# Optimization experiments

Measured on AMD Instinct MI355X. Metric: run time of the kernel, lower is better.

The kernel has to match this reference:

```python
import jax, jax.numpy as jnp
import numpy as np


def setup_inputs() -> dict:
    key = jax.random.key(0)
    ks = jax.random.split(key, 8)
    B, I, H = 4096, 2048, 2048
    C = I + H
    s = 1.0 / np.sqrt(C)
    return {
        "x": jax.random.normal(ks[0], (B, I), jnp.float32),
        "h": jax.random.normal(ks[1], (B, H), jnp.float32),
        "W_update": jax.random.normal(ks[2], (H, C), jnp.float32) * s,
        "b_update": jax.random.normal(ks[3], (H,), jnp.float32) * s,
        "W_select": jax.random.normal(ks[4], (H, C), jnp.float32) * s,
        "b_select": jax.random.normal(ks[5], (H,), jnp.float32) * s,
        "W_predict": jax.random.normal(ks[6], (H, C), jnp.float32) * s,
        "b_predict": jax.random.normal(ks[7], (H,), jnp.float32) * s,
    }


def reference(x, h, W_update, b_update, W_select, b_select, W_predict, b_predict):
    # combined = [x, h]  -> [B, I+H]
    combined = jnp.concatenate([x, h], axis=1)
    to_update = jax.nn.sigmoid(combined @ W_update.T + b_update)  # [B, H]
    to_select = jax.nn.sigmoid(combined @ W_select.T + b_select)  # [B, H]
    updated = h * to_update
    new_combined = jnp.concatenate([x, updated], axis=1)
    predictions = jnp.tanh(new_combined @ W_predict.T + b_predict)
    selected = predictions * to_select
    h_new = h * (1.0 - to_select) + selected
    return h_new
```

## Files before the change

kernel.cpp:

```cpp
#include <hip/hip_runtime.h>
#include <stdint.h>

#define IDIM 2048
#define HDIM 2048
#define CDIM 4096
#define BDIM 4096
#define KDIM 4096

typedef float f32x4 __attribute__((ext_vector_type(4)));
typedef short s16x8 __attribute__((ext_vector_type(8)));
typedef unsigned short u16;
typedef u16 u16x8 __attribute__((ext_vector_type(8)));

__device__ __forceinline__ u16 f2bf(float f) {
    union { float f; uint32_t u; } v; v.f = f;
    uint32_t r = v.u + 0x7fffu + ((v.u >> 16) & 1u);
    return (u16)(r >> 16);
}

__device__ __forceinline__ u16x8 cvt8(float4 v0, float4 v1) {
    u16x8 o;
    o[0] = f2bf(v0.x); o[1] = f2bf(v0.y); o[2] = f2bf(v0.z); o[3] = f2bf(v0.w);
    o[4] = f2bf(v1.x); o[5] = f2bf(v1.y); o[6] = f2bf(v1.z); o[7] = f2bf(v1.w);
    return o;
}

__device__ __forceinline__ void gload_lds16(const void* g, void* l) {
    __builtin_amdgcn_global_load_lds(
        (__attribute__((address_space(1))) void*)g,
        (__attribute__((address_space(3))) void*)l,
        16, 0, 0);
}

__global__ void prep_kernel(const float* __restrict__ x, const float* __restrict__ h,
                            const float* __restrict__ Wu, const float* __restrict__ Ws,
                            u16* __restrict__ comb, u16* __restrict__ newc,
                            u16* __restrict__ wpack) {
    const int WCNT = (HDIM * CDIM) / 8;
    int i = blockIdx.x * blockDim.x + threadIdx.x;
    if (i < 2 * WCNT) {
        const float* src = (i < WCNT) ? Wu : Ws;
        const int g = (i < WCNT) ? i : i - WCNT;
        u16* dst = wpack + (i < WCNT ? (size_t)0 : (size_t)HDIM * CDIM);
        const float4* s4 = (const float4*)src;
        ((u16x8*)dst)[g] = cvt8(s4[2 * g], s4[2 * g + 1]);
    } else {
        const int p = i - 2 * WCNT;
        const int b = p >> 9;
        const int c = (p & 511) * 8;
        const float* src = (c < IDIM) ? (x + (size_t)b * IDIM + c)
                                      : (h + (size_t)b * HDIM + (c - IDIM));
        u16x8 o = cvt8(((const float4*)src)[0], ((const float4*)src)[1]);
        *(u16x8*)(comb + (size_t)b * CDIM + c) = o;
        if (c < IDIM) *(u16x8*)(newc + (size_t)b * CDIM + c) = o;
    }
}

__global__ void gemm_bt1(const u16* __restrict__ A, const u16* __restrict__ Bm,
                         const float* __restrict__ h,
                         const float* __restrict__ bias0, const float* __restrict__ bias1,
                         float* __restrict__ Sout, u16* __restrict__ newc,
                         const float* __restrict__ Wp, u16* __restrict__ wpred) {
    constexpr int BM = 128, BK = 64;
    const int tid  = threadIdx.x;
    const int lane = tid & 63;
    const int wave = tid >> 6;
    const int wr = wave >> 1, wc = wave & 1;
    const int bm = blockIdx.y * BM;
    const int bn = blockIdx.x * BM;

    __shared__ __align__(16) u16 lA[BM * BK];
    __shared__ __align__(16) u16 lB[BM * BK];

    f32x4 acc[4][4] = {};

    const int srow = wave * 32 + (lane >> 3);
    const int sg   = (lane & 7) ^ (lane >> 3);

    auto stage = [&](int k0) {
        #pragma unroll
        for (int i = 0; i < 4; ++i) {
            const int r = srow + i * 8;
            gload_lds16(A  + (size_t)(bm + r) * KDIM + k0 + sg * 8,
                        &lA[(wave * 32 + i * 8) * 64]);
            gload_lds16(Bm + (size_t)(bn + r) * KDIM + k0 + sg * 8,
                        &lB[(wave * 32 + i * 8) * 64]);
        }
    };

    stage(0);
    constexpr int NT = KDIM / BK;
    for (int kt = 0; kt < NT; ++kt) {
        __syncthreads();
        #pragma unroll
        for (int ks = 0; ks < 2; ++ks) {
            s16x8 af[4], bfr[4];
            #pragma unroll
            for (int m = 0; m < 4; ++m) {
                const int row = wr * 64 + m * 16 + (lane & 15);
                const int j   = ks * 4 + (lane >> 4);
                af[m] = *(const s16x8*)&lA[row * 64 + ((j ^ (row & 7)) << 3)];
            }
            #pragma unroll
            for (int n = 0; n < 4; ++n) {
                const int row = wc * 64 + n * 16 + (lane & 15);
                const int j   = ks * 4 + (lane >> 4);
                bfr[n] = *(const s16x8*)&lB[row * 64 + ((j ^ (row & 7)) << 3)];
            }
            #pragma unroll
            for (int m = 0; m < 4; ++m)
                #pragma unroll
                for (int n = 0; n < 4; ++n)
                    acc[m][n] = __builtin_amdgcn_mfma_f32_16x16x32_bf16(
                        af[m], bfr[n], acc[m][n], 0, 0, 0);
        }
        __syncthreads();
        if (kt + 1 < NT) stage((kt + 1) * BK);
    }

    #pragma unroll
    for (int m = 0; m < 4; ++m) {
        const int r0 = bm + wr * 64 + m * 16 + ((lane >> 4) << 2);
        #pragma unroll
        for (int n = 0; n < 4; ++n) {
            const int col = bn + wc * 64 + n * 16 + (lane & 15);
            #pragma unroll
            for (int j = 0; j < 4; ++j) {
                const int r = r0 + j;
                const float v = acc[m][n][j];
                const float bv = (col < HDIM) ? bias0[col] : bias1[col - HDIM];
                const float sgm = 1.0f / (1.0f + __expf(-(v + bv)));
                if (col < HDIM) {
                    const float hv = h[(size_t)r * HDIM + col];
                    newc[(size_t)r * CDIM + IDIM + col] = f2bf(hv * sgm);
                } else {
                    Sout[(size_t)r * HDIM + (col - HDIM)] = sgm;
                }
            }
        }
    }

    {
        const int bid = blockIdx.y * (CDIM / 128) + blockIdx.x;
        const size_t base = (size_t)bid * 8192;
        const float4* s4 = (const float4*)(Wp + base);
        u16x8* d8 = (u16x8*)(wpred + base);
        #pragma unroll
        for (int t = 0; t < 4; ++t) {
            const int g = t * 256 + tid;
            d8[g] = cvt8(s4[2 * g], s4[2 * g + 1]);
        }
    }
}

__global__ __launch_bounds__(128, 3) void gemm_bt2(
        const u16* __restrict__ A, const u16* __restrict__ Bm,
        const float* __restrict__ h, const float* __restrict__ bias0,
        float* __restrict__ Sout) {
    constexpr int BM = 128, BN = 64, BK = 64;
    const int tid  = threadIdx.x;
    const int lane = tid & 63;
    const int wave = tid >> 6;
    const int bm = blockIdx.y * BM;
    const int bn = blockIdx.x * BN;

    __shared__ __align__(16) u16 lA[BM * BK];
    __shared__ __align__(16) u16 lB[BN * BK];

    f32x4 acc[4][4] = {};

    const int srow = tid >> 3;
    const int ssw  = ((tid & 7) ^ (srow & 7)) << 3;

    auto stage = [&](int k0) {
        #pragma unroll
        for (int c = 0; c < 8; ++c)
            gload_lds16(A + (size_t)(bm + c * 16 + srow) * KDIM + k0 + ssw,
                        &lA[(c * 16 + wave * 8) * 64]);
        #pragma unroll
        for (int c = 0; c < 4; ++c)
            gload_lds16(Bm + (size_t)(bn + c * 16 + srow) * KDIM + k0 + ssw,
                        &lB[(c * 16 + wave * 8) * 64]);
    };

    stage(0);
    constexpr int NT = KDIM / BK;
    for (int kt = 0; kt < NT; ++kt) {
        __syncthreads();
        #pragma unroll
        for (int ks = 0; ks < 2; ++ks) {
            s16x8 af[4], bfr[4];
            #pragma unroll
            for (int m = 0; m < 4; ++m) {
                const int row = wave * 64 + m * 16 + (lane & 15);
                const int j   = ks * 4 + (lane >> 4);
                af[m] = *(const s16x8*)&lA[row * 64 + ((j ^ (row & 7)) << 3)];
            }
            #pragma unroll
            for (int n = 0; n < 4; ++n) {
                const int row = n * 16 + (lane & 15);
                const int j   = ks * 4 + (lane >> 4);
                bfr[n] = *(const s16x8*)&lB[row * 64 + ((j ^ (row & 7)) << 3)];
            }
            #pragma unroll
            for (int m = 0; m < 4; ++m)
                #pragma unroll
                for (int n = 0; n < 4; ++n)
                    acc[m][n] = __builtin_amdgcn_mfma_f32_16x16x32_bf16(
                        af[m], bfr[n], acc[m][n], 0, 0, 0);
        }
        __syncthreads();
        if (kt + 1 < NT) stage((kt + 1) * BK);
    }

    #pragma unroll
    for (int m = 0; m < 4; ++m) {
        const int r0 = bm + wave * 64 + m * 16 + ((lane >> 4) << 2);
        #pragma unroll
        for (int n = 0; n < 4; ++n) {
            const int col = bn + n * 16 + (lane & 15);
            #pragma unroll
            for (int j = 0; j < 4; ++j) {
                const int r = r0 + j;
                const float p = tanhf(acc[m][n][j] + bias0[col]);
                const size_t idx = (size_t)r * HDIM + col;
                const float s  = Sout[idx];
                const float hv = h[idx];
                Sout[idx] = hv * (1.0f - s) + p * s;
            }
        }
    }
}

extern "C" void kernel_launch(void* const* d_in, const int* in_sizes, int n_in,
                              void* d_out, int out_size, void* d_ws, size_t ws_size,
                              hipStream_t stream) {
    (void)in_sizes; (void)n_in; (void)out_size; (void)ws_size;
    const float* x  = (const float*)d_in[0];
    const float* h  = (const float*)d_in[1];
    const float* Wu = (const float*)d_in[2];
    const float* bu = (const float*)d_in[3];
    const float* Ws = (const float*)d_in[4];
    const float* bs = (const float*)d_in[5];
    const float* Wp = (const float*)d_in[6];
    const float* bp = (const float*)d_in[7];
    float* out = (float*)d_out;

    u16* comb  = (u16*)d_ws;
    u16* newc  = comb  + (size_t)BDIM * CDIM;
    u16* wpack = newc  + (size_t)BDIM * CDIM;
    u16* wpred = wpack + (size_t)2 * HDIM * CDIM;

    const int ngrp = 2 * ((HDIM * CDIM) / 8) + (BDIM * CDIM) / 8;
    prep_kernel<<<ngrp / 256, 256, 0, stream>>>(x, h, Wu, Ws, comb, newc, wpack);

    gemm_bt1<<<dim3(CDIM / 128, BDIM / 128), 256, 0, stream>>>(
        comb, wpack, h, bu, bs, out, newc, Wp, wpred);
    gemm_bt2<<<dim3(HDIM / 64, BDIM / 128), 128, 0, stream>>>(
        newc, wpred, h, bp, out);
}
```

Measured before the change: 290.2 us.

## Move Wp conversion into prep kernel and use 2-wave 128x128 tiles in gemm1

The bf16 conversion of W_predict moves out of the first GEMM's epilogue and into the prep kernel, whose weight branch now handles three matrices. wpred still points at the third slot of wpack, so gemm_bt2 reads the same data as before. The first GEMM drops from four waves to two per 128x128 tile, so each wave computes a 64x128 sub-tile with 32 accumulators and reuses each A fragment across eight B fragments. The intent is more MFMA work per LDS read and a GEMM that no longer carries the conversion tail, at the cost of higher register pressure and fewer waves available to hide latency.

```diff
diff --git a/kernel.cpp b/kernel.cpp
--- a/kernel.cpp
+++ b/kernel.cpp
@@ -34,18 +34,20 @@
 
 __global__ void prep_kernel(const float* __restrict__ x, const float* __restrict__ h,
                             const float* __restrict__ Wu, const float* __restrict__ Ws,
+                            const float* __restrict__ Wp,
                             u16* __restrict__ comb, u16* __restrict__ newc,
                             u16* __restrict__ wpack) {
     const int WCNT = (HDIM * CDIM) / 8;
     int i = blockIdx.x * blockDim.x + threadIdx.x;
-    if (i < 2 * WCNT) {
-        const float* src = (i < WCNT) ? Wu : Ws;
-        const int g = (i < WCNT) ? i : i - WCNT;
-        u16* dst = wpack + (i < WCNT ? (size_t)0 : (size_t)HDIM * CDIM);
+    if (i < 3 * WCNT) {
+        const float* src; size_t off; int g;
+        if (i < WCNT)          { src = Wu; off = 0;                        g = i; }
+        else if (i < 2 * WCNT) { src = Ws; off = (size_t)HDIM * CDIM;      g = i - WCNT; }
+        else                   { src = Wp; off = (size_t)2 * HDIM * CDIM;  g = i - 2 * WCNT; }
         const float4* s4 = (const float4*)src;
-        ((u16x8*)dst)[g] = cvt8(s4[2 * g], s4[2 * g + 1]);
+        ((u16x8*)(wpack + off))[g] = cvt8(s4[2 * g], s4[2 * g + 1]);
     } else {
-        const int p = i - 2 * WCNT;
+        const int p = i - 3 * WCNT;
         const int b = p >> 9;
         const int c = (p & 511) * 8;
         const float* src = (c < IDIM) ? (x + (size_t)b * IDIM + c)
@@ -56,36 +58,35 @@
     }
 }
 
-__global__ void gemm_bt1(const u16* __restrict__ A, const u16* __restrict__ Bm,
-                         const float* __restrict__ h,
-                         const float* __restrict__ bias0, const float* __restrict__ bias1,
-                         float* __restrict__ Sout, u16* __restrict__ newc,
-                         const float* __restrict__ Wp, u16* __restrict__ wpred) {
-    constexpr int BM = 128, BK = 64;
+__global__ __launch_bounds__(128, 2) void gemm_bt1(
+        const u16* __restrict__ A, const u16* __restrict__ Bm,
+        const float* __restrict__ h,
+        const float* __restrict__ bias0, const float* __restrict__ bias1,
+        float* __restrict__ Sout, u16* __restrict__ newc) {
+    constexpr int BM = 128, BN = 128, BK = 64;
     const int tid  = threadIdx.x;
     const int lane = tid & 63;
     const int wave = tid >> 6;
-    const int wr = wave >> 1, wc = wave & 1;
     const int bm = blockIdx.y * BM;
-    const int bn = blockIdx.x * BM;
+    const int bn = blockIdx.x * BN;
 
     __shared__ __align__(16) u16 lA[BM * BK];
-    __shared__ __align__(16) u16 lB[BM * BK];
-
-    f32x4 acc[4][4] = {};
-
-    const int srow = wave * 32 + (lane >> 3);
-    const int sg   = (lane & 7) ^ (lane >> 3);
+    __shared__ __align__(16) u16 lB[BN * BK];
+
+    f32x4 acc[4][8] = {};
+
+    const int srow = tid >> 3;
+    const int ssw  = ((tid & 7) ^ (srow & 7)) << 3;
 
     auto stage = [&](int k0) {
         #pragma unroll
-        for (int i = 0; i < 4; ++i) {
-            const int r = srow + i * 8;
-            gload_lds16(A  + (size_t)(bm + r) * KDIM + k0 + sg * 8,
-                        &lA[(wave * 32 + i * 8) * 64]);
-            gload_lds16(Bm + (size_t)(bn + r) * KDIM + k0 + sg * 8,
-                        &lB[(wave * 32 + i * 8) * 64]);
-        }
+        for (int c = 0; c < 8; ++c)
+            gload_lds16(A + (size_t)(bm + c * 16 + srow) * KDIM + k0 + ssw,
+                        &lA[(c * 16 + wave * 8) * 64]);
+        #pragma unroll
+        for (int c = 0; c < 8; ++c)
+            gload_lds16(Bm + (size_t)(bn + c * 16 + srow) * KDIM + k0 + ssw,
+                        &lB[(c * 16 + wave * 8) * 64]);
     };
 
     stage(0);
@@ -94,23 +95,23 @@
         __syncthreads();
         #pragma unroll
         for (int ks = 0; ks < 2; ++ks) {
-            s16x8 af[4], bfr[4];
+            s16x8 af[4], bfr[8];
             #pragma unroll
             for (int m = 0; m < 4; ++m) {
-                const int row = wr * 64 + m * 16 + (lane & 15);
+                const int row = wave * 64 + m * 16 + (lane & 15);
                 const int j   = ks * 4 + (lane >> 4);
                 af[m] = *(const s16x8*)&lA[row * 64 + ((j ^ (row & 7)) << 3)];
             }
             #pragma unroll
-            for (int n = 0; n < 4; ++n) {
-                const int row = wc * 64 + n * 16 + (lane & 15);
+            for (int n = 0; n < 8; ++n) {
+                const int row = n * 16 + (lane & 15);
                 const int j   = ks * 4 + (lane >> 4);
                 bfr[n] = *(const s16x8*)&lB[row * 64 + ((j ^ (row & 7)) << 3)];
             }
             #pragma unroll
             for (int m = 0; m < 4; ++m)
                 #pragma unroll
-                for (int n = 0; n < 4; ++n)
+                for (int n = 0; n < 8; ++n)
                     acc[m][n] = __builtin_amdgcn_mfma_f32_16x16x32_bf16(
                         af[m], bfr[n], acc[m][n], 0, 0, 0);
         }
@@ -120,10 +121,10 @@
 
     #pragma unroll
     for (int m = 0; m < 4; ++m) {
-        const int r0 = bm + wr * 64 + m * 16 + ((lane >> 4) << 2);
-        #pragma unroll
-        for (int n = 0; n < 4; ++n) {
-            const int col = bn + wc * 64 + n * 16 + (lane & 15);
+        const int r0 = bm + wave * 64 + m * 16 + ((lane >> 4) << 2);
+        #pragma unroll
+        for (int n = 0; n < 8; ++n) {
+            const int col = bn + n * 16 + (lane & 15);
             #pragma unroll
             for (int j = 0; j < 4; ++j) {
                 const int r = r0 + j;
@@ -137,18 +138,6 @@
                     Sout[(size_t)r * HDIM + (col - HDIM)] = sgm;
                 }
             }
-        }
-    }
-
-    {
-        const int bid = blockIdx.y * (CDIM / 128) + blockIdx.x;
-        const size_t base = (size_t)bid * 8192;
-        const float4* s4 = (const float4*)(Wp + base);
-        u16x8* d8 = (u16x8*)(wpred + base);
-        #pragma unroll
-        for (int t = 0; t < 4; ++t) {
-            const int g = t * 256 + tid;
-            d8[g] = cvt8(s4[2 * g], s4[2 * g + 1]);
         }
     }
 }
@@ -251,11 +240,11 @@
     u16* wpack = newc  + (size_t)BDIM * CDIM;
     u16* wpred = wpack + (size_t)2 * HDIM * CDIM;
 
-    const int ngrp = 2 * ((HDIM * CDIM) / 8) + (BDIM * CDIM) / 8;
-    prep_kernel<<<ngrp / 256, 256, 0, stream>>>(x, h, Wu, Ws, comb, newc, wpack);
-
-    gemm_bt1<<<dim3(CDIM / 128, BDIM / 128), 256, 0, stream>>>(
-        comb, wpack, h, bu, bs, out, newc, Wp, wpred);
+    const int ngrp = 3 * ((HDIM * CDIM) / 8) + (BDIM * CDIM) / 8;
+    prep_kernel<<<ngrp / 256, 256, 0, stream>>>(x, h, Wu, Ws, Wp, comb, newc, wpack);
+
+    gemm_bt1<<<dim3(CDIM / 128, BDIM / 128), 128, 0, stream>>>(
+        comb, wpack, h, bu, bs, out, newc);
     gemm_bt2<<<dim3(HDIM / 64, BDIM / 128), 128, 0, stream>>>(
         newc, wpred, h, bp, out);
 }
```

Result: slower. 304.5 us (+4.9%).

## Cut intermediate traffic: bf16 gate buffer, split updated-h buffer, move Wp conversion to prep

Applied to the files above, without the earlier changes.

Stops writing a duplicate x half into a separate new-combined buffer. The second GEMM now reads its A operand from the combined buffer for the x columns and from a compact updated-h buffer for the rest. The select gate is stored as bf16 instead of fp32, and h is read back from the bf16 combined buffer instead of the fp32 input, which lowers precision for the final blend. Wp conversion moves from the gemm1 epilogue into the prep kernel.

```diff
diff --git a/kernel.cpp b/kernel.cpp
--- a/kernel.cpp
+++ b/kernel.cpp
@@ -18,6 +18,11 @@
     return (u16)(r >> 16);
 }
 
+__device__ __forceinline__ float b2f(u16 b) {
+    union { uint32_t u; float f; } v; v.u = ((uint32_t)b) << 16;
+    return v.f;
+}
+
 __device__ __forceinline__ u16x8 cvt8(float4 v0, float4 v1) {
     u16x8 o;
     o[0] = f2bf(v0.x); o[1] = f2bf(v0.y); o[2] = f2bf(v0.z); o[3] = f2bf(v0.w);
@@ -34,33 +39,31 @@
 
 __global__ void prep_kernel(const float* __restrict__ x, const float* __restrict__ h,
                             const float* __restrict__ Wu, const float* __restrict__ Ws,
-                            u16* __restrict__ comb, u16* __restrict__ newc,
-                            u16* __restrict__ wpack) {
+                            const float* __restrict__ Wp,
+                            u16* __restrict__ comb, u16* __restrict__ wpack) {
     const int WCNT = (HDIM * CDIM) / 8;
     int i = blockIdx.x * blockDim.x + threadIdx.x;
-    if (i < 2 * WCNT) {
-        const float* src = (i < WCNT) ? Wu : Ws;
-        const int g = (i < WCNT) ? i : i - WCNT;
-        u16* dst = wpack + (i < WCNT ? (size_t)0 : (size_t)HDIM * CDIM);
+    if (i < 3 * WCNT) {
+        const float* src; size_t off; int g;
+        if (i < WCNT)          { src = Wu; off = 0;                        g = i; }
+        else if (i < 2 * WCNT) { src = Ws; off = (size_t)HDIM * CDIM;      g = i - WCNT; }
+        else                   { src = Wp; off = (size_t)2 * HDIM * CDIM;  g = i - 2 * WCNT; }
         const float4* s4 = (const float4*)src;
-        ((u16x8*)dst)[g] = cvt8(s4[2 * g], s4[2 * g + 1]);
+        ((u16x8*)(wpack + off))[g] = cvt8(s4[2 * g], s4[2 * g + 1]);
     } else {
-        const int p = i - 2 * WCNT;
+        const int p = i - 3 * WCNT;
         const int b = p >> 9;
         const int c = (p & 511) * 8;
         const float* src = (c < IDIM) ? (x + (size_t)b * IDIM + c)
                                       : (h + (size_t)b * HDIM + (c - IDIM));
         u16x8 o = cvt8(((const float4*)src)[0], ((const float4*)src)[1]);
         *(u16x8*)(comb + (size_t)b * CDIM + c) = o;
-        if (c < IDIM) *(u16x8*)(newc + (size_t)b * CDIM + c) = o;
     }
 }
 
 __global__ void gemm_bt1(const u16* __restrict__ A, const u16* __restrict__ Bm,
-                         const float* __restrict__ h,
                          const float* __restrict__ bias0, const float* __restrict__ bias1,
-                         float* __restrict__ Sout, u16* __restrict__ newc,
-                         const float* __restrict__ Wp, u16* __restrict__ wpred) {
+                         u16* __restrict__ upd, u16* __restrict__ S) {
     constexpr int BM = 128, BK = 64;
     const int tid  = threadIdx.x;
     const int lane = tid & 63;
@@ -131,32 +134,20 @@
                 const float bv = (col < HDIM) ? bias0[col] : bias1[col - HDIM];
                 const float sgm = 1.0f / (1.0f + __expf(-(v + bv)));
                 if (col < HDIM) {
-                    const float hv = h[(size_t)r * HDIM + col];
-                    newc[(size_t)r * CDIM + IDIM + col] = f2bf(hv * sgm);
+                    const float hv = b2f(A[(size_t)r * CDIM + IDIM + col]);
+                    upd[(size_t)r * HDIM + col] = f2bf(hv * sgm);
                 } else {
-                    Sout[(size_t)r * HDIM + (col - HDIM)] = sgm;
+                    S[(size_t)r * HDIM + (col - HDIM)] = f2bf(sgm);
                 }
             }
         }
     }
-
-    {
-        const int bid = blockIdx.y * (CDIM / 128) + blockIdx.x;
-        const size_t base = (size_t)bid * 8192;
-        const float4* s4 = (const float4*)(Wp + base);
-        u16x8* d8 = (u16x8*)(wpred + base);
-        #pragma unroll
-        for (int t = 0; t < 4; ++t) {
-            const int g = t * 256 + tid;
-            d8[g] = cvt8(s4[2 * g], s4[2 * g + 1]);
-        }
-    }
 }
 
 __global__ __launch_bounds__(128, 3) void gemm_bt2(
-        const u16* __restrict__ A, const u16* __restrict__ Bm,
-        const float* __restrict__ h, const float* __restrict__ bias0,
-        float* __restrict__ Sout) {
+        const u16* __restrict__ comb, const u16* __restrict__ upd,
+        const u16* __restrict__ Bm, const float* __restrict__ bias0,
+        const u16* __restrict__ S, float* __restrict__ out) {
     constexpr int BM = 128, BN = 64, BK = 64;
     const int tid  = threadIdx.x;
     const int lane = tid & 63;
@@ -173,10 +164,14 @@
     const int ssw  = ((tid & 7) ^ (srow & 7)) << 3;
 
     auto stage = [&](int k0) {
-        #pragma unroll
-        for (int c = 0; c < 8; ++c)
-            gload_lds16(A + (size_t)(bm + c * 16 + srow) * KDIM + k0 + ssw,
-                        &lA[(c * 16 + wave * 8) * 64]);
+        const bool inX = (k0 < IDIM);
+        #pragma unroll
+        for (int c = 0; c < 8; ++c) {
+            const int r = bm + c * 16 + srow;
+            const u16* src = inX ? (comb + (size_t)r * CDIM + k0 + ssw)
+                                 : (upd  + (size_t)r * HDIM + (k0 - IDIM) + ssw);
+            gload_lds16(src, &lA[(c * 16 + wave * 8) * 64]);
+        }
         #pragma unroll
         for (int c = 0; c < 4; ++c)
             gload_lds16(Bm + (size_t)(bn + c * 16 + srow) * KDIM + k0 + ssw,
@@ -224,9 +219,9 @@
                 const int r = r0 + j;
                 const float p = tanhf(acc[m][n][j] + bias0[col]);
                 const size_t idx = (size_t)r * HDIM + col;
-                const float s  = Sout[idx];
-                const float hv = h[idx];
-                Sout[idx] = hv * (1.0f - s) + p * s;
+                const float s  = b2f(S[idx]);
+                const float hv = b2f(comb[(size_t)r * CDIM + IDIM + col]);
+                out[idx] = hv * (1.0f - s) + p * s;
             }
         }
     }
@@ -247,15 +242,16 @@
     float* out = (float*)d_out;
 
     u16* comb  = (u16*)d_ws;
-    u16* newc  = comb  + (size_t)BDIM * CDIM;
-    u16* wpack = newc  + (size_t)BDIM * CDIM;
+    u16* wpack = comb  + (size_t)BDIM * CDIM;
     u16* wpred = wpack + (size_t)2 * HDIM * CDIM;
-
-    const int ngrp = 2 * ((HDIM * CDIM) / 8) + (BDIM * CDIM) / 8;
-    prep_kernel<<<ngrp / 256, 256, 0, stream>>>(x, h, Wu, Ws, comb, newc, wpack);
+    u16* upd   = wpack + (size_t)3 * HDIM * CDIM;
+    u16* S     = upd   + (size_t)BDIM * HDIM;
+
+    const int ngrp = 3 * ((HDIM * CDIM) / 8) + (BDIM * CDIM) / 8;
+    prep_kernel<<<ngrp / 256, 256, 0, stream>>>(x, h, Wu, Ws, Wp, comb, wpack);
 
     gemm_bt1<<<dim3(CDIM / 128, BDIM / 128), 256, 0, stream>>>(
-        comb, wpack, h, bu, bs, out, newc, Wp, wpred);
+        comb, wpack, bu, bs, upd, S);
     gemm_bt2<<<dim3(HDIM / 64, BDIM / 128), 128, 0, stream>>>(
-        newc, wpred, h, bp, out);
-}
+        comb, upd, wpred, bp, S, out);
+}
```

Measured after the change: 285.8 us, median of 2. About the same (-1.5%).
